# Kernel optimization log

Hardware: AMD Instinct MI355X
Metric: run time of the kernel (lower is better)

Reference implementation:

```python
import jax, jax.numpy as jnp
import numpy as np

B, T, S, H = 4, 128, 512, 512


def setup_inputs() -> dict:
    key = jax.random.key(0)
    k1, k2, k3, k4, k5, k6, k7 = jax.random.split(key, 7)
    query = jax.random.normal(k1, (B, T, H), dtype=jnp.float32)
    encoder_outputs = jax.random.normal(k2, (B, S, H), dtype=jnp.float32)
    src_lengths = jax.random.randint(k3, (B,), 1, S + 1)
    src_lengths = src_lengths.at[0].set(S)  # torch code assumes max(len) == S
    scale = 1.0 / np.sqrt(H)
    W_h = jax.random.normal(k4, (H, H), dtype=jnp.float32) * scale
    W_s = jax.random.normal(k5, (H, H), dtype=jnp.float32) * scale
    v = jax.random.normal(k6, (H,), dtype=jnp.float32) * scale
    W_out = jax.random.normal(k7, (2 * H, H), dtype=jnp.float32) * scale
    return {"query": query, "encoder_outputs": encoder_outputs,
            "src_lengths": src_lengths, "W_h": W_h, "W_s": W_s,
            "v": v, "W_out": W_out}


def reference(query, encoder_outputs, src_lengths, W_h, W_s, v, W_out):
    # Project once, then broadcast (same math as torch's Linear on expanded tensors)
    pq = jnp.einsum('bth,hk->btk', query, W_s)            # (B,T,H) : W_s applied to query
    pe = jnp.einsum('bsh,hk->bsk', encoder_outputs, W_h)  # (B,S,H) : W_h applied to encoder
    # score(h_i, s_j) = v^T tanh(W_s q + W_h e)
    score = jnp.einsum('btsh,h->bts', jnp.tanh(pq[:, :, None, :] + pe[:, None, :, :]), v)  # (B,T,S)
    mask = (jnp.arange(score.shape[-1]) [None, :] < src_lengths[:, None])[:, None, :]  # (B,1,S)
    score = jnp.where(mask, score, -jnp.inf)
    alignment = jax.nn.softmax(score, axis=-1)            # (B,T,S)
    context = jnp.einsum('bts,bsh->bth', alignment, encoder_outputs)  # (B,T,H)
    attn_out = jnp.tanh(jnp.concatenate([context, query], axis=-1) @ W_out)  # (B,T,H)
    return attn_out
```

## Files before the change

kernel.cpp:

```cpp
#include <hip/hip_runtime.h>
#include <math.h>

#define HD 512
#define BB 4
#define TT 128
#define SS 512

typedef __attribute__((ext_vector_type(8))) short short8;
typedef __attribute__((ext_vector_type(4))) float floatx4;
typedef _Float16 half2_t __attribute__((ext_vector_type(2)));
typedef unsigned short ushort_t;
typedef unsigned int uint_t;

__device__ __forceinline__ float tanh_e(float x) {
    float t = __builtin_amdgcn_rcpf(__expf(2.f * x) + 1.f);
    return fmaf(-2.f, t, 1.f);
}
__device__ __forceinline__ ushort_t f2bf(float x) {
    unsigned int u = __float_as_uint(x);
    u += 0x7fffu + ((u >> 16) & 1u);
    return (ushort_t)(u >> 16);
}

__global__ __launch_bounds__(256) void wtrans_kernel(
    const float* __restrict__ Ws, const float* __restrict__ Wh,
    const float* __restrict__ Wo, const float* __restrict__ query,
    const float* __restrict__ enc,
    ushort_t* __restrict__ Ts, ushort_t* __restrict__ Th, ushort_t* __restrict__ To,
    ushort_t* __restrict__ cq, ushort_t* __restrict__ encB)
{
    const int bid = blockIdx.x;
    const int tid = threadIdx.x;
    if (bid < 128) {
        const float* src; ushort_t* dst; int K, l;
        if (bid < 32)      { src = Ws; dst = Ts; K = 512;  l = bid;      }
        else if (bid < 64) { src = Wh; dst = Th; K = 512;  l = bid - 32; }
        else               { src = Wo; dst = To; K = 1024; l = bid - 64; }
        const int ktiles = K >> 7;
        const int tk = l & (ktiles - 1), tn = l / ktiles;
        const int k0 = tk * 128, n0 = tn * 64;

        __shared__ ushort_t tile[64][136];

        const int lr  = tid >> 4;
        const int lc4 = (tid & 15) * 4;
        #pragma unroll
        for (int p = 0; p < 8; ++p) {
            const int row = p * 16 + lr;
            float4 s = *(const float4*)(src + (size_t)(k0 + row) * HD + n0 + lc4);
            tile[lc4 + 0][row] = f2bf(s.x);
            tile[lc4 + 1][row] = f2bf(s.y);
            tile[lc4 + 2][row] = f2bf(s.z);
            tile[lc4 + 3][row] = f2bf(s.w);
        }
        __syncthreads();
        const int n = tid >> 2, kc = (tid & 3) * 32;
        #pragma unroll
        for (int j = 0; j < 4; ++j) {
            uint4 o = *(const uint4*)&tile[n][kc + j * 8];
            *(uint4*)&dst[(size_t)(n0 + n) * K + k0 + kc + j * 8] = o;
        }
    } else if (bid < 256) {
        const int idx = ((bid - 128) * 256 + tid) * 8;
        const int m = idx >> 9, h = idx & 511;
        float4 q0 = *(const float4*)(query + (size_t)m * HD + h);
        float4 q1 = *(const float4*)(query + (size_t)m * HD + h + 4);
        uint4 o;
        o.x = (uint_t)f2bf(q0.x) | ((uint_t)f2bf(q0.y) << 16);
        o.y = (uint_t)f2bf(q0.z) | ((uint_t)f2bf(q0.w) << 16);
        o.z = (uint_t)f2bf(q1.x) | ((uint_t)f2bf(q1.y) << 16);
        o.w = (uint_t)f2bf(q1.z) | ((uint_t)f2bf(q1.w) << 16);
        *(uint4*)&cq[(size_t)m * 1024 + 512 + h] = o;
    } else {
        const size_t idx = ((size_t)(bid - 256) * 256 + tid) * 8;
        float4 e0 = *(const float4*)(enc + idx);
        float4 e1 = *(const float4*)(enc + idx + 4);
        uint4 o;
        o.x = (uint_t)f2bf(e0.x) | ((uint_t)f2bf(e0.y) << 16);
        o.y = (uint_t)f2bf(e0.z) | ((uint_t)f2bf(e0.w) << 16);
        o.z = (uint_t)f2bf(e1.x) | ((uint_t)f2bf(e1.y) << 16);
        o.w = (uint_t)f2bf(e1.z) | ((uint_t)f2bf(e1.w) << 16);
        *(uint4*)&encB[idx] = o;
    }
}

#define LDP 40
__global__ __launch_bounds__(256) void proj_kernel(
    const ushort_t* __restrict__ cq, const ushort_t* __restrict__ encB,
    const ushort_t* __restrict__ WTs, const ushort_t* __restrict__ WTh,
    const float* __restrict__ v,
    float2* __restrict__ tqa, _Float16* __restrict__ peT)
{
    const int bm = blockIdx.x;
    const int bn = blockIdx.y;
    const bool isQ = (bm < 8);
    const ushort_t* A = isQ ? (cq + 512) : encB;
    const int lda = isQ ? 1024 : 512;
    const ushort_t* WT = isQ ? WTs : WTh;
    const int m0 = (isQ ? bm : bm - 8) * 64;
    const int n0 = bn * 64;

    __shared__ ushort_t As[64 * LDP];
    __shared__ ushort_t Bs[64 * LDP];

    const int tid = threadIdx.x;
    const int lane = tid & 63, w = tid >> 6;
    const int quad = lane >> 4, lrow = lane & 15;
    const int mw = (w & 1) * 32, nw = (w >> 1) * 32;

    const int ar = tid >> 2;
    const int ac = (tid & 3) * 8;

    floatx4 zero = {0.f, 0.f, 0.f, 0.f};
    floatx4 acc[2][2] = {{zero, zero}, {zero, zero}};

    uint4 ald = *(const uint4*)&A[(size_t)(m0 + ar) * lda + ac];
    uint4 bld = *(const uint4*)&WT[(size_t)(n0 + ar) * HD + ac];

    for (int k0 = 0; k0 < HD; k0 += 32) {
        __syncthreads();
        *(uint4*)&As[ar * LDP + ac] = ald;
        *(uint4*)&Bs[ar * LDP + ac] = bld;
        __syncthreads();
        if (k0 + 32 < HD) {
            ald = *(const uint4*)&A[(size_t)(m0 + ar) * lda + k0 + 32 + ac];
            bld = *(const uint4*)&WT[(size_t)(n0 + ar) * HD + k0 + 32 + ac];
        }
        short8 af[2], bf[2];
        #pragma unroll
        for (int i = 0; i < 2; ++i)
            af[i] = *(const short8*)&As[(mw + i * 16 + lrow) * LDP + quad * 8];
        #pragma unroll
        for (int j = 0; j < 2; ++j)
            bf[j] = *(const short8*)&Bs[(nw + j * 16 + lrow) * LDP + quad * 8];
        #pragma unroll
        for (int i = 0; i < 2; ++i)
            #pragma unroll
            for (int j = 0; j < 2; ++j)
                acc[i][j] = __builtin_amdgcn_mfma_f32_16x16x32_bf16(af[i], bf[j], acc[i][j], 0, 0, 0);
    }

    if (isQ) {
        #pragma unroll
        for (int j = 0; j < 2; ++j) {
            const int col = n0 + nw + j * 16 + lrow;
            const float vj = v[col];
            #pragma unroll
            for (int i = 0; i < 2; ++i)
                #pragma unroll
                for (int r = 0; r < 4; ++r) {
                    const int row = m0 + mw + i * 16 + quad * 4 + r;
                    float tq = tanh_e(acc[i][j][r]);
                    float2 o; o.x = tq; o.y = vj * tq;
                    tqa[(size_t)row * HD + col] = o;
                }
        }
    } else {
        #pragma unroll
        for (int i = 0; i < 2; ++i)
            #pragma unroll
            for (int j = 0; j < 2; ++j) {
                const int gm = m0 + mw + i * 16 + quad * 4;
                const int b = gm >> 9, s = gm & 511;
                const int col = n0 + nw + j * 16 + lrow;
                _Float16 t0 = (_Float16)tanh_e(acc[i][j][0]);
                _Float16 t1 = (_Float16)tanh_e(acc[i][j][1]);
                _Float16 t2 = (_Float16)tanh_e(acc[i][j][2]);
                _Float16 t3 = (_Float16)tanh_e(acc[i][j][3]);
                ushort4 o;
                o.x = *(ushort_t*)&t0; o.y = *(ushort_t*)&t1;
                o.z = *(ushort_t*)&t2; o.w = *(ushort_t*)&t3;
                *(ushort4*)((ushort_t*)peT + ((size_t)b * HD + col) * SS + s) = o;
            }
    }
}

__global__ __launch_bounds__(128) void score_part_kernel(
    const float2* __restrict__ tqa, const _Float16* __restrict__ peT,
    const float* __restrict__ vv, const int* __restrict__ lens,
    _Float16* __restrict__ sp)
{
    const int bt = blockIdx.x;
    const int hq = blockIdx.y;
    const int b = bt >> 7;
    const int tid = threadIdx.x;
    const int h0 = hq * 128;

    const int len = lens[b];
    const int s0 = tid * 4;
    if (s0 >= len) return;

    const float2* qa = tqa + (size_t)bt * HD + h0;
    const float* vp = vv + h0;
    const ushort_t* col = (const ushort_t*)peT + ((size_t)b * HD + h0) * SS + s0;

    float acc[4] = {0.f, 0.f, 0.f, 0.f};
    #pragma unroll 4
    for (int h = 0; h < 128; h += 2) {
        uint2 pA = *(const uint2*)(col + (size_t)h * SS);
        uint2 pB = *(const uint2*)(col + (size_t)(h + 1) * SS);
        const float2 qA = qa[h], qB = qa[h + 1];
        const float vA = vp[h], vB = vp[h + 1];
        half2_t a01 = *(half2_t*)&pA.x, a23 = *(half2_t*)&pA.y;
        half2_t b01 = *(half2_t*)&pB.x, b23 = *(half2_t*)&pB.y;
        float teA[4] = {(float)a01[0], (float)a01[1], (float)a23[0], (float)a23[1]};
        float teB[4] = {(float)b01[0], (float)b01[1], (float)b23[0], (float)b23[1]};
        #pragma unroll
        for (int s = 0; s < 4; ++s) {
            float dA = fmaf(qA.x, teA[s], 1.f);
            float dB = fmaf(qB.x, teB[s], 1.f);
            float mA = fmaf(vA, teA[s], qA.y);
            float mB = fmaf(vB, teB[s], qB.y);
            float num = mA * dB;
            num = fmaf(mB, dA, num);
            acc[s] = fmaf(num, __builtin_amdgcn_rcpf(dA * dB), acc[s]);
        }
    }
    _Float16 f0 = (_Float16)acc[0], f1 = (_Float16)acc[1];
    _Float16 f2 = (_Float16)acc[2], f3 = (_Float16)acc[3];
    uint2 pk;
    pk.x = (uint_t)*(ushort_t*)&f0 | ((uint_t)*(ushort_t*)&f1 << 16);
    pk.y = (uint_t)*(ushort_t*)&f2 | ((uint_t)*(ushort_t*)&f3 << 16);
    *(uint2*)(sp + ((size_t)hq * (BB * TT) + bt) * SS + s0) = pk;
}

__global__ __launch_bounds__(512) void combine_kernel(
    const _Float16* __restrict__ sp, const int* __restrict__ lens,
    float* __restrict__ alpha)
{
    const int bt = blockIdx.x;
    const int b = bt >> 7;
    const int tid = threadIdx.x;
    const int wave = tid >> 6;
    __shared__ float s_red[16];

    const int len = lens[b];
    float sc = -INFINITY;
    if (tid < len) {
        const size_t i = (size_t)bt * SS + tid;
        const size_t st = (size_t)BB * TT * SS;
        sc = (float)sp[i] + (float)sp[i + st] + (float)sp[i + 2 * st] + (float)sp[i + 3 * st];
    }
    float m = sc;
    #pragma unroll
    for (int off = 32; off; off >>= 1) m = fmaxf(m, __shfl_xor(m, off, 64));
    if ((tid & 63) == 0) s_red[wave] = m;
    __syncthreads();
    m = s_red[0];
    #pragma unroll
    for (int w2 = 1; w2 < 8; ++w2) m = fmaxf(m, s_red[w2]);

    float e = (tid < len) ? __expf(sc - m) : 0.f;
    float sum = e;
    #pragma unroll
    for (int off = 32; off; off >>= 1) sum += __shfl_xor(sum, off, 64);
    if ((tid & 63) == 0) s_red[8 + wave] = sum;
    __syncthreads();
    float total = s_red[8];
    #pragma unroll
    for (int w2 = 1; w2 < 8; ++w2) total += s_red[8 + w2];

    alpha[(size_t)bt * SS + tid] = e * __builtin_amdgcn_rcpf(total);
}

#define LDA_A 40
#define LDA_B 76
__global__ __launch_bounds__(256) void ctx_kernel(
    const float* __restrict__ alpha, const ushort_t* __restrict__ encB,
    const int* __restrict__ lens, ushort_t* __restrict__ cq)
{
    const int b = blockIdx.x;
    const int t0 = blockIdx.y * 16;
    const int h0 = blockIdx.z * 64;
    __shared__ ushort_t sA[16 * LDA_A];
    __shared__ ushort_t sB[32 * LDA_B];
    const int tid = threadIdx.x;
    const int lane = tid & 63, w = tid >> 6;
    const int quad = lane >> 4, lrow = lane & 15;
    const int nw = w * 16;
    const int len = lens[b];

    const int ar  = tid >> 4;
    const int ac2 = (tid & 15) * 2;
    const int br  = tid >> 3;
    const int bc8 = (tid & 7) * 8;

    floatx4 acc = {0.f, 0.f, 0.f, 0.f};

    for (int s0 = 0; s0 < len; s0 += 32) {
        __syncthreads();
        {
            float2 a2 = *(const float2*)(alpha + (size_t)(b * TT + t0 + ar) * SS + s0 + ac2);
            uint_t pk = (uint_t)f2bf(a2.x) | ((uint_t)f2bf(a2.y) << 16);
            *(uint_t*)&sA[ar * LDA_A + ac2] = pk;
            uint4 ev = *(const uint4*)&encB[(size_t)(b * SS + s0 + br) * HD + h0 + bc8];
            *(uint4*)&sB[br * LDA_B + bc8] = ev;
        }
        __syncthreads();
        short8 af = *(const short8*)&sA[lrow * LDA_A + quad * 8];
        short8 bf;
        #pragma unroll
        for (int j = 0; j < 8; ++j)
            bf[j] = (short)sB[(quad * 8 + j) * LDA_B + nw + lrow];
        acc = __builtin_amdgcn_mfma_f32_16x16x32_bf16(af, bf, acc, 0, 0, 0);
    }
    #pragma unroll
    for (int r = 0; r < 4; ++r)
        cq[(size_t)(b * TT + t0 + quad * 4 + r) * 1024 + h0 + nw + lrow] = f2bf(acc[r]);
}

__global__ __launch_bounds__(256) void out_kernel(
    const ushort_t* __restrict__ cq, const ushort_t* __restrict__ WTo,
    float* __restrict__ out)
{
    const int m0 = blockIdx.x * 32;
    const int n0 = blockIdx.y * 32;

    __shared__ ushort_t As[32 * LDP];
    __shared__ ushort_t Bs[32 * LDP];

    const int tid = threadIdx.x;
    const int lane = tid & 63, w = tid >> 6;
    const int quad = lane >> 4, lrow = lane & 15;
    const int mw = (w & 1) * 16, nw = (w >> 1) * 16;

    const int r8 = tid >> 3, c4 = (tid & 7) * 4;

    floatx4 acc = {0.f, 0.f, 0.f, 0.f};

    uint2 av = *(const uint2*)&cq[(size_t)(m0 + r8) * 1024 + c4];
    uint2 bv = *(const uint2*)&WTo[(size_t)(n0 + r8) * 1024 + c4];

    for (int k0 = 0; k0 < 1024; k0 += 32) {
        __syncthreads();
        *(uint2*)&As[r8 * LDP + c4] = av;
        *(uint2*)&Bs[r8 * LDP + c4] = bv;
        __syncthreads();
        if (k0 + 32 < 1024) {
            av = *(const uint2*)&cq[(size_t)(m0 + r8) * 1024 + k0 + 32 + c4];
            bv = *(const uint2*)&WTo[(size_t)(n0 + r8) * 1024 + k0 + 32 + c4];
        }
        short8 af = *(const short8*)&As[(mw + lrow) * LDP + quad * 8];
        short8 bf = *(const short8*)&Bs[(nw + lrow) * LDP + quad * 8];
        acc = __builtin_amdgcn_mfma_f32_16x16x32_bf16(af, bf, acc, 0, 0, 0);
    }
    #pragma unroll
    for (int r = 0; r < 4; ++r) {
        const int row = m0 + mw + quad * 4 + r;
        const int col = n0 + nw + lrow;
        out[(size_t)row * HD + col] = tanh_e(acc[r]);
    }
}

extern "C" void kernel_launch(void* const* d_in, const int* in_sizes, int n_in,
                              void* d_out, int out_size, void* d_ws, size_t ws_size,
                              hipStream_t stream) {
    (void)in_sizes; (void)n_in; (void)out_size; (void)ws_size;
    const float* query = (const float*)d_in[0];
    const float* enc   = (const float*)d_in[1];
    const int*   lens  = (const int*)d_in[2];
    const float* W_h   = (const float*)d_in[3];
    const float* W_s   = (const float*)d_in[4];
    const float* v     = (const float*)d_in[5];
    const float* W_out = (const float*)d_in[6];
    float* out = (float*)d_out;

    ushort_t* WTs   = (ushort_t*)d_ws;
    ushort_t* WTh   = WTs + (size_t)HD * HD;
    ushort_t* WTo   = WTh + (size_t)HD * HD;
    ushort_t* encB  = WTo + (size_t)HD * 2 * HD;
    float2*   tqa   = (float2*)(encB + (size_t)BB * SS * HD);
    _Float16* peT   = (_Float16*)(tqa + (size_t)BB * TT * HD);
    _Float16* sp    = peT + (size_t)BB * HD * SS;
    float*    alpha = (float*)(sp + (size_t)4 * BB * TT * SS);
    ushort_t* cq    = (ushort_t*)(alpha + (size_t)BB * TT * SS);

    wtrans_kernel<<<dim3(768), 256, 0, stream>>>(W_s, W_h, W_out, query, enc,
                                                 WTs, WTh, WTo, cq, encB);
    proj_kernel<<<dim3(40, 8), 256, 0, stream>>>(cq, encB, WTs, WTh, v, tqa, peT);
    score_part_kernel<<<dim3(BB * TT, 4), 128, 0, stream>>>(tqa, peT, v, lens, sp);
    combine_kernel<<<dim3(BB * TT), 512, 0, stream>>>(sp, lens, alpha);
    ctx_kernel<<<dim3(BB, TT / 16, HD / 64), 256, 0, stream>>>(alpha, encB, lens, cq);
    out_kernel<<<dim3(16, 16), 256, 0, stream>>>(cq, WTo, out);
}
```

Measured before the change: 125.7 us.

## Precompute enc@W_out and query@W_out, fuse score, softmax and output

Uses associativity to precompute encoder_outputs·W_out[:H] and query·W_out[H:] in the projection kernel. A single per-(b,t) fused kernel then computes scores, softmax and alpha·encWo plus tanh directly. This removes the partial-score, combine, context and output kernels and their intermediate buffers. In exchange, score work is spread over only 512 blocks covering all H per block, and a larger fp16 encWo buffer is stored and read through strided 4-byte loads.

New measurement: 151.8 us. 20.7% more time.

```diff
diff --git a/kernel.cpp b/kernel.cpp
--- a/kernel.cpp
+++ b/kernel.cpp
@@ -88,16 +88,17 @@
 __global__ __launch_bounds__(256) void proj_kernel(
     const ushort_t* __restrict__ cq, const ushort_t* __restrict__ encB,
     const ushort_t* __restrict__ WTs, const ushort_t* __restrict__ WTh,
-    const float* __restrict__ v,
-    float2* __restrict__ tqa, _Float16* __restrict__ peT)
+    const ushort_t* __restrict__ WTo, const float* __restrict__ v,
+    float2* __restrict__ tqa, _Float16* __restrict__ peT,
+    _Float16* __restrict__ encWo, float* __restrict__ qWob)
 {
     const int bm = blockIdx.x;
     const int bn = blockIdx.y;
-    const bool isQ = (bm < 8);
-    const ushort_t* A = isQ ? (cq + 512) : encB;
-    const int lda = isQ ? 1024 : 512;
-    const ushort_t* WT = isQ ? WTs : WTh;
-    const int m0 = (isQ ? bm : bm - 8) * 64;
+    int type; const ushort_t* A; int lda; const ushort_t* B; int ldb; int m0;
+    if (bm < 8)       { type = 0; A = cq + 512; lda = 1024; B = WTs;       ldb = 512;  m0 = bm * 64;        }
+    else if (bm < 40) { type = 1; A = encB;     lda = 512;  B = WTh;       ldb = 512;  m0 = (bm - 8) * 64;  }
+    else if (bm < 72) { type = 2; A = encB;     lda = 512;  B = WTo;       ldb = 1024; m0 = (bm - 40) * 64; }
+    else              { type = 3; A = cq + 512; lda = 1024; B = WTo + 512; ldb = 1024; m0 = (bm - 72) * 64; }
     const int n0 = bn * 64;
 
     __shared__ ushort_t As[64 * LDP];
@@ -115,7 +116,7 @@
     floatx4 acc[2][2] = {{zero, zero}, {zero, zero}};
 
     uint4 ald = *(const uint4*)&A[(size_t)(m0 + ar) * lda + ac];
-    uint4 bld = *(const uint4*)&WT[(size_t)(n0 + ar) * HD + ac];
+    uint4 bld = *(const uint4*)&B[(size_t)(n0 + ar) * ldb + ac];
 
     for (int k0 = 0; k0 < HD; k0 += 32) {
         __syncthreads();
@@ -124,7 +125,7 @@
         __syncthreads();
         if (k0 + 32 < HD) {
             ald = *(const uint4*)&A[(size_t)(m0 + ar) * lda + k0 + 32 + ac];
-            bld = *(const uint4*)&WT[(size_t)(n0 + ar) * HD + k0 + 32 + ac];
+            bld = *(const uint4*)&B[(size_t)(n0 + ar) * ldb + k0 + 32 + ac];
         }
         short8 af[2], bf[2];
         #pragma unroll
@@ -140,7 +141,7 @@
                 acc[i][j] = __builtin_amdgcn_mfma_f32_16x16x32_bf16(af[i], bf[j], acc[i][j], 0, 0, 0);
     }
 
-    if (isQ) {
+    if (type == 0) {
         #pragma unroll
         for (int j = 0; j < 2; ++j) {
             const int col = n0 + nw + j * 16 + lrow;
@@ -155,7 +156,7 @@
                     tqa[(size_t)row * HD + col] = o;
                 }
         }
-    } else {
+    } else if (type == 1) {
         #pragma unroll
         for (int i = 0; i < 2; ++i)
             #pragma unroll
@@ -172,184 +173,127 @@
                 o.z = *(ushort_t*)&t2; o.w = *(ushort_t*)&t3;
                 *(ushort4*)((ushort_t*)peT + ((size_t)b * HD + col) * SS + s) = o;
             }
-    }
-}
-
-__global__ __launch_bounds__(128) void score_part_kernel(
+    } else if (type == 2) {
+        #pragma unroll
+        for (int i = 0; i < 2; ++i)
+            #pragma unroll
+            for (int j = 0; j < 2; ++j) {
+                const int col = n0 + nw + j * 16 + lrow;
+                #pragma unroll
+                for (int r = 0; r < 4; ++r) {
+                    const int gm = m0 + mw + i * 16 + quad * 4 + r;
+                    encWo[(size_t)gm * HD + col] = (_Float16)acc[i][j][r];
+                }
+            }
+    } else {
+        #pragma unroll
+        for (int i = 0; i < 2; ++i)
+            #pragma unroll
+            for (int j = 0; j < 2; ++j) {
+                const int col = n0 + nw + j * 16 + lrow;
+                #pragma unroll
+                for (int r = 0; r < 4; ++r) {
+                    const int gm = m0 + mw + i * 16 + quad * 4 + r;
+                    qWob[(size_t)gm * HD + col] = acc[i][j][r];
+                }
+            }
+    }
+}
+
+__global__ __launch_bounds__(256) void fused_kernel(
     const float2* __restrict__ tqa, const _Float16* __restrict__ peT,
-    const float* __restrict__ vv, const int* __restrict__ lens,
-    _Float16* __restrict__ sp)
-{
-    const int bt = blockIdx.x;
-    const int hq = blockIdx.y;
-    const int b = bt >> 7;
-    const int tid = threadIdx.x;
-    const int h0 = hq * 128;
-
-    const int len = lens[b];
-    const int s0 = tid * 4;
-    if (s0 >= len) return;
-
-    const float2* qa = tqa + (size_t)bt * HD + h0;
-    const float* vp = vv + h0;
-    const ushort_t* col = (const ushort_t*)peT + ((size_t)b * HD + h0) * SS + s0;
-
-    float acc[4] = {0.f, 0.f, 0.f, 0.f};
-    #pragma unroll 4
-    for (int h = 0; h < 128; h += 2) {
-        uint2 pA = *(const uint2*)(col + (size_t)h * SS);
-        uint2 pB = *(const uint2*)(col + (size_t)(h + 1) * SS);
-        const float2 qA = qa[h], qB = qa[h + 1];
-        const float vA = vp[h], vB = vp[h + 1];
-        half2_t a01 = *(half2_t*)&pA.x, a23 = *(half2_t*)&pA.y;
-        half2_t b01 = *(half2_t*)&pB.x, b23 = *(half2_t*)&pB.y;
-        float teA[4] = {(float)a01[0], (float)a01[1], (float)a23[0], (float)a23[1]};
-        float teB[4] = {(float)b01[0], (float)b01[1], (float)b23[0], (float)b23[1]};
-        #pragma unroll
-        for (int s = 0; s < 4; ++s) {
-            float dA = fmaf(qA.x, teA[s], 1.f);
-            float dB = fmaf(qB.x, teB[s], 1.f);
-            float mA = fmaf(vA, teA[s], qA.y);
-            float mB = fmaf(vB, teB[s], qB.y);
-            float num = mA * dB;
-            num = fmaf(mB, dA, num);
-            acc[s] = fmaf(num, __builtin_amdgcn_rcpf(dA * dB), acc[s]);
-        }
-    }
-    _Float16 f0 = (_Float16)acc[0], f1 = (_Float16)acc[1];
-    _Float16 f2 = (_Float16)acc[2], f3 = (_Float16)acc[3];
-    uint2 pk;
-    pk.x = (uint_t)*(ushort_t*)&f0 | ((uint_t)*(ushort_t*)&f1 << 16);
-    pk.y = (uint_t)*(ushort_t*)&f2 | ((uint_t)*(ushort_t*)&f3 << 16);
-    *(uint2*)(sp + ((size_t)hq * (BB * TT) + bt) * SS + s0) = pk;
-}
-
-__global__ __launch_bounds__(512) void combine_kernel(
-    const _Float16* __restrict__ sp, const int* __restrict__ lens,
-    float* __restrict__ alpha)
+    const float* __restrict__ vv, const _Float16* __restrict__ encWo,
+    const float* __restrict__ qWob, const int* __restrict__ lens,
+    float* __restrict__ out)
 {
     const int bt = blockIdx.x;
     const int b = bt >> 7;
     const int tid = threadIdx.x;
-    const int wave = tid >> 6;
-    __shared__ float s_red[16];
-
+    const int lane = tid & 63, wid = tid >> 6;
     const int len = lens[b];
-    float sc = -INFINITY;
-    if (tid < len) {
-        const size_t i = (size_t)bt * SS + tid;
-        const size_t st = (size_t)BB * TT * SS;
-        sc = (float)sp[i] + (float)sp[i + st] + (float)sp[i + 2 * st] + (float)sp[i + 3 * st];
-    }
-    float m = sc;
+    const int s0 = tid * 2;
+
+    __shared__ float s_alpha[SS];
+    __shared__ float s_red[8];
+
+    float acc0 = 0.f, acc1 = 0.f;
+    if (s0 < len) {
+        const float2* qa = tqa + (size_t)bt * HD;
+        const float* vp = vv;
+        const ushort_t* col = (const ushort_t*)peT + (size_t)b * HD * SS + s0;
+        #pragma unroll 4
+        for (int h = 0; h < HD; h += 2) {
+            uint_t pA = *(const uint_t*)(col + (size_t)h * SS);
+            uint_t pB = *(const uint_t*)(col + (size_t)(h + 1) * SS);
+            const float2 qA = qa[h], qB = qa[h + 1];
+            const float vA = vp[h], vB = vp[h + 1];
+            half2_t a01 = *(half2_t*)&pA;
+            half2_t b01 = *(half2_t*)&pB;
+            float teA0 = (float)a01[0], teA1 = (float)a01[1];
+            float teB0 = (float)b01[0], teB1 = (float)b01[1];
+            float dA0 = fmaf(qA.x, teA0, 1.f);
+            float dB0 = fmaf(qB.x, teB0, 1.f);
+            float mA0 = fmaf(vA, teA0, qA.y);
+            float mB0 = fmaf(vB, teB0, qB.y);
+            float num0 = mA0 * dB0;
+            num0 = fmaf(mB0, dA0, num0);
+            acc0 = fmaf(num0, __builtin_amdgcn_rcpf(dA0 * dB0), acc0);
+            float dA1 = fmaf(qA.x, teA1, 1.f);
+            float dB1 = fmaf(qB.x, teB1, 1.f);
+            float mA1 = fmaf(vA, teA1, qA.y);
+            float mB1 = fmaf(vB, teB1, qB.y);
+            float num1 = mA1 * dB1;
+            num1 = fmaf(mB1, dA1, num1);
+            acc1 = fmaf(num1, __builtin_amdgcn_rcpf(dA1 * dB1), acc1);
+        }
+    }
+    float sc0 = (s0     < len) ? acc0 : -INFINITY;
+    float sc1 = (s0 + 1 < len) ? acc1 : -INFINITY;
+
+    float m = fmaxf(sc0, sc1);
     #pragma unroll
     for (int off = 32; off; off >>= 1) m = fmaxf(m, __shfl_xor(m, off, 64));
-    if ((tid & 63) == 0) s_red[wave] = m;
+    if (lane == 0) s_red[wid] = m;
     __syncthreads();
-    m = s_red[0];
-    #pragma unroll
-    for (int w2 = 1; w2 < 8; ++w2) m = fmaxf(m, s_red[w2]);
-
-    float e = (tid < len) ? __expf(sc - m) : 0.f;
-    float sum = e;
+    m = fmaxf(fmaxf(s_red[0], s_red[1]), fmaxf(s_red[2], s_red[3]));
+
+    float e0 = __expf(sc0 - m);
+    float e1 = __expf(sc1 - m);
+    float sum = e0 + e1;
     #pragma unroll
     for (int off = 32; off; off >>= 1) sum += __shfl_xor(sum, off, 64);
-    if ((tid & 63) == 0) s_red[8 + wave] = sum;
+    if (lane == 0) s_red[4 + wid] = sum;
     __syncthreads();
-    float total = s_red[8];
-    #pragma unroll
-    for (int w2 = 1; w2 < 8; ++w2) total += s_red[8 + w2];
-
-    alpha[(size_t)bt * SS + tid] = e * __builtin_amdgcn_rcpf(total);
-}
-
-#define LDA_A 40
-#define LDA_B 76
-__global__ __launch_bounds__(256) void ctx_kernel(
-    const float* __restrict__ alpha, const ushort_t* __restrict__ encB,
-    const int* __restrict__ lens, ushort_t* __restrict__ cq)
-{
-    const int b = blockIdx.x;
-    const int t0 = blockIdx.y * 16;
-    const int h0 = blockIdx.z * 64;
-    __shared__ ushort_t sA[16 * LDA_A];
-    __shared__ ushort_t sB[32 * LDA_B];
-    const int tid = threadIdx.x;
-    const int lane = tid & 63, w = tid >> 6;
-    const int quad = lane >> 4, lrow = lane & 15;
-    const int nw = w * 16;
-    const int len = lens[b];
-
-    const int ar  = tid >> 4;
-    const int ac2 = (tid & 15) * 2;
-    const int br  = tid >> 3;
-    const int bc8 = (tid & 7) * 8;
-
-    floatx4 acc = {0.f, 0.f, 0.f, 0.f};
-
-    for (int s0 = 0; s0 < len; s0 += 32) {
-        __syncthreads();
-        {
-            float2 a2 = *(const float2*)(alpha + (size_t)(b * TT + t0 + ar) * SS + s0 + ac2);
-            uint_t pk = (uint_t)f2bf(a2.x) | ((uint_t)f2bf(a2.y) << 16);
-            *(uint_t*)&sA[ar * LDA_A + ac2] = pk;
-            uint4 ev = *(const uint4*)&encB[(size_t)(b * SS + s0 + br) * HD + h0 + bc8];
-            *(uint4*)&sB[br * LDA_B + bc8] = ev;
-        }
-        __syncthreads();
-        short8 af = *(const short8*)&sA[lrow * LDA_A + quad * 8];
-        short8 bf;
-        #pragma unroll
-        for (int j = 0; j < 8; ++j)
-            bf[j] = (short)sB[(quad * 8 + j) * LDA_B + nw + lrow];
-        acc = __builtin_amdgcn_mfma_f32_16x16x32_bf16(af, bf, acc, 0, 0, 0);
-    }
-    #pragma unroll
-    for (int r = 0; r < 4; ++r)
-        cq[(size_t)(b * TT + t0 + quad * 4 + r) * 1024 + h0 + nw + lrow] = f2bf(acc[r]);
-}
-
-__global__ __launch_bounds__(256) void out_kernel(
-    const ushort_t* __restrict__ cq, const ushort_t* __restrict__ WTo,
-    float* __restrict__ out)
-{
-    const int m0 = blockIdx.x * 32;
-    const int n0 = blockIdx.y * 32;
-
-    __shared__ ushort_t As[32 * LDP];
-    __shared__ ushort_t Bs[32 * LDP];
-
-    const int tid = threadIdx.x;
-    const int lane = tid & 63, w = tid >> 6;
-    const int quad = lane >> 4, lrow = lane & 15;
-    const int mw = (w & 1) * 16, nw = (w >> 1) * 16;
-
-    const int r8 = tid >> 3, c4 = (tid & 7) * 4;
-
-    floatx4 acc = {0.f, 0.f, 0.f, 0.f};
-
-    uint2 av = *(const uint2*)&cq[(size_t)(m0 + r8) * 1024 + c4];
-    uint2 bv = *(const uint2*)&WTo[(size_t)(n0 + r8) * 1024 + c4];
-
-    for (int k0 = 0; k0 < 1024; k0 += 32) {
-        __syncthreads();
-        *(uint2*)&As[r8 * LDP + c4] = av;
-        *(uint2*)&Bs[r8 * LDP + c4] = bv;
-        __syncthreads();
-        if (k0 + 32 < 1024) {
-            av = *(const uint2*)&cq[(size_t)(m0 + r8) * 1024 + k0 + 32 + c4];
-            bv = *(const uint2*)&WTo[(size_t)(n0 + r8) * 1024 + k0 + 32 + c4];
-        }
-        short8 af = *(const short8*)&As[(mw + lrow) * LDP + quad * 8];
-        short8 bf = *(const short8*)&Bs[(nw + lrow) * LDP + quad * 8];
-        acc = __builtin_amdgcn_mfma_f32_16x16x32_bf16(af, bf, acc, 0, 0, 0);
-    }
-    #pragma unroll
-    for (int r = 0; r < 4; ++r) {
-        const int row = m0 + mw + quad * 4 + r;
-        const int col = n0 + nw + lrow;
-        out[(size_t)row * HD + col] = tanh_e(acc[r]);
-    }
+    float total = (s_red[4] + s_red[5]) + (s_red[6] + s_red[7]);
+    float inv = __builtin_amdgcn_rcpf(total);
+    s_alpha[s0]     = e0 * inv;
+    s_alpha[s0 + 1] = e1 * inv;
+    __syncthreads();
+
+    const int n0 = s0;
+    float2 qb = *(const float2*)(qWob + (size_t)bt * HD + n0);
+    float p0a = qb.x, p0b = 0.f, p0c = 0.f, p0d = 0.f;
+    float p1a = qb.y, p1b = 0.f, p1c = 0.f, p1d = 0.f;
+    const ushort_t* ew = (const ushort_t*)encWo + (size_t)b * SS * HD + n0;
+    const int lenR = (len + 3) & ~3;
+    for (int s = 0; s < lenR; s += 4) {
+        uint_t w0 = *(const uint_t*)(ew + (size_t)(s + 0) * HD);
+        uint_t w1 = *(const uint_t*)(ew + (size_t)(s + 1) * HD);
+        uint_t w2 = *(const uint_t*)(ew + (size_t)(s + 2) * HD);
+        uint_t w3 = *(const uint_t*)(ew + (size_t)(s + 3) * HD);
+        float a0 = s_alpha[s], a1 = s_alpha[s + 1];
+        float a2 = s_alpha[s + 2], a3 = s_alpha[s + 3];
+        half2_t h0 = *(half2_t*)&w0, h1 = *(half2_t*)&w1;
+        half2_t h2 = *(half2_t*)&w2, h3 = *(half2_t*)&w3;
+        p0a = fmaf(a0, (float)h0[0], p0a); p1a = fmaf(a0, (float)h0[1], p1a);
+        p0b = fmaf(a1, (float)h1[0], p0b); p1b = fmaf(a1, (float)h1[1], p1b);
+        p0c = fmaf(a2, (float)h2[0], p0c); p1c = fmaf(a2, (float)h2[1], p1c);
+        p0d = fmaf(a3, (float)h3[0], p0d); p1d = fmaf(a3, (float)h3[1], p1d);
+    }
+    float o0 = (p0a + p0b) + (p0c + p0d);
+    float o1 = (p1a + p1b) + (p1c + p1d);
+    float2 ov; ov.x = tanh_e(o0); ov.y = tanh_e(o1);
+    *(float2*)(out + (size_t)bt * HD + n0) = ov;
 }
 
 extern "C" void kernel_launch(void* const* d_in, const int* in_sizes, int n_in,
@@ -371,15 +315,13 @@
     ushort_t* encB  = WTo + (size_t)HD * 2 * HD;
     float2*   tqa   = (float2*)(encB + (size_t)BB * SS * HD);
     _Float16* peT   = (_Float16*)(tqa + (size_t)BB * TT * HD);
-    _Float16* sp    = peT + (size_t)BB * HD * SS;
-    float*    alpha = (float*)(sp + (size_t)4 * BB * TT * SS);
-    ushort_t* cq    = (ushort_t*)(alpha + (size_t)BB * TT * SS);
+    _Float16* encWo = peT + (size_t)BB * HD * SS;
+    float*    qWob  = (float*)(encWo + (size_t)BB * SS * HD);
+    ushort_t* cq    = (ushort_t*)(qWob + (size_t)BB * TT * HD);
 
     wtrans_kernel<<<dim3(768), 256, 0, stream>>>(W_s, W_h, W_out, query, enc,
                                                  WTs, WTh, WTo, cq, encB);
-    proj_kernel<<<dim3(40, 8), 256, 0, stream>>>(cq, encB, WTs, WTh, v, tqa, peT);
-    score_part_kernel<<<dim3(BB * TT, 4), 128, 0, stream>>>(tqa, peT, v, lens, sp);
-    combine_kernel<<<dim3(BB * TT), 512, 0, stream>>>(sp, lens, alpha);
-    ctx_kernel<<<dim3(BB, TT / 16, HD / 64), 256, 0, stream>>>(alpha, encB, lens, cq);
-    out_kernel<<<dim3(16, 16), 256, 0, stream>>>(cq, WTo, out);
-}
+    proj_kernel<<<dim3(80, 8), 256, 0, stream>>>(cq, encB, WTs, WTh, WTo, v,
+                                                 tqa, peT, encWo, qWob);
+    fused_kernel<<<dim3(BB * TT), 256, 0, stream>>>(tqa, peT, v, encWo, qWob, lens, out);
+}
```
